# Kernel optimization log

Hardware: AMD Instinct MI355X
Metric: run time of the kernel (lower is better)

The kernel has to match this reference:

```python
import jax, jax.numpy as jnp
import numpy as np

B, T, E, H = 2, 2048, 1024, 16
HS = E // H  # head_size = 64
EPS = 1e-5


def _layernorm(x, g, b):
    mu = jnp.mean(x, axis=-1, keepdims=True)
    var = jnp.mean(jnp.square(x - mu), axis=-1, keepdims=True)
    return (x - mu) * jax.lax.rsqrt(var + EPS) * g + b


def _block_forward(x, wq, wk, wv, wp, bp, ln1_g, ln1_b, ln2_g, ln2_b,
                   w1, b1, w2, b2, w3, b3, wg_att, bg_att, wg_ff, bg_ff):
    Bc, Tc, Ec = x.shape
    # --- multi-head causal self-attention on ln1(x) ---
    h = _layernorm(x, ln1_g, ln1_b)
    q = jnp.einsum('bte,hek->bhtk', h, wq)  # [B,H,T,HS]
    k = jnp.einsum('bte,hek->bhtk', h, wk)
    v = jnp.einsum('bte,hek->bhtk', h, wv)
    scores = jnp.einsum('bhtk,bhsk->bhts', q, k) * (HS ** -0.5)
    causal = jnp.tril(jnp.ones((Tc, Tc), dtype=bool))
    scores = jnp.where(causal, scores, jnp.finfo(scores.dtype).min)
    wei = jax.nn.softmax(scores, axis=-1)  # [B,H,T,T] (returned, as in torch)
    attn = jnp.einsum('bhts,bhsk->bhtk', wei, v)
    # concat heads in head order -> [B,T,H*HS]
    attn = attn.transpose(0, 2, 1, 3).reshape(Bc, Tc, H * HS)
    sa_out = attn @ wp + bp
    # gated residual: gate from new value, multiply residual (old x)
    gate = jax.nn.sigmoid(sa_out @ wg_att + bg_att)
    x = sa_out + gate * x
    # --- feed-forward on ln2(x) ---
    h2 = _layernorm(x, ln2_g, ln2_b)
    f = jax.nn.gelu(h2 @ w1 + b1, approximate=False)   # [B,T,4E]
    f = jax.nn.gelu(f @ w2 + b2, approximate=False)    # [B,T,2E]
    f = f @ w3 + b3                                     # [B,T,E]
    gate2 = jax.nn.sigmoid(f @ wg_ff + bg_ff)
    x = f + gate2 * x
    return x, wei


def setup_inputs() -> dict:
    key = jax.random.key(0)
    ks = jax.random.split(key, 24)
    s = 0.02
    n = lambda i, shape: (jax.random.normal(ks[i], shape) * s).astype(jnp.float32)
    return {
        'x': jax.random.normal(ks[0], (B, T, E), dtype=jnp.float32),
        'wq': n(1, (H, E, HS)), 'wk': n(2, (H, E, HS)), 'wv': n(3, (H, E, HS)),
        'wp': n(4, (H * HS, E)), 'bp': jnp.zeros((E,), jnp.float32),
        'ln1_g': jnp.ones((E,), jnp.float32), 'ln1_b': jnp.zeros((E,), jnp.float32),
        'ln2_g': jnp.ones((E,), jnp.float32), 'ln2_b': jnp.zeros((E,), jnp.float32),
        'w1': n(5, (E, 4 * E)), 'b1': jnp.zeros((4 * E,), jnp.float32),
        'w2': n(6, (4 * E, 2 * E)), 'b2': jnp.zeros((2 * E,), jnp.float32),
        'w3': n(7, (2 * E, E)), 'b3': jnp.zeros((E,), jnp.float32),
        'wg_att': n(8, (E, E)), 'bg_att': jnp.zeros((E,), jnp.float32),
        'wg_ff': n(9, (E, E)), 'bg_ff': jnp.zeros((E,), jnp.float32),
    }


def reference(x, wq, wk, wv, wp, bp, ln1_g, ln1_b, ln2_g, ln2_b,
              w1, b1, w2, b2, w3, b3, wg_att, bg_att, wg_ff, bg_ff):
    return _block_forward(x, wq, wk, wv, wp, bp, ln1_g, ln1_b, ln2_g, ln2_b,
                          w1, b1, w2, b2, w3, b3, wg_att, bg_att, wg_ff, bg_ff)
```

## Files before the change

kernel.cpp:

```cpp
#include <hip/hip_runtime.h>
#include <hip/hip_bf16.h>

typedef unsigned short u16;
typedef __attribute__((ext_vector_type(8))) short short8;
typedef __attribute__((ext_vector_type(4))) float floatx4;

#define DI __device__ __forceinline__

constexpr int Tn  = 2048;
constexpr int En  = 1024;
constexpr int BTn = 4096;

DI float bf2f(u16 u) { union { unsigned int i; float f; } v; v.i = (unsigned int)u << 16; return v.f; }
DI u16 f2bf(float f) {
  union { float f; unsigned int i; } u; u.f = f;
  unsigned int r = u.i + 0x7FFFu + ((u.i >> 16) & 1u);
  return (u16)(r >> 16);
}
DI float gelu_f(float x) { return 0.5f * x * (1.f + erff(x * 0.70710678118654752f)); }
DI float sigmoid_f(float x) { return 1.f / (1.f + __expf(-x)); }

DI void gload_lds16(const u16* g, u16* l) {
  __builtin_amdgcn_global_load_lds(
      (const __attribute__((address_space(1))) unsigned int*)g,
      (__attribute__((address_space(3))) unsigned int*)l, 16, 0, 0);
}

template <int EPI>
__launch_bounds__(256, 2)
__global__ void gemm_bt(const u16* __restrict__ A, const u16* __restrict__ Bt,
                        const float* __restrict__ bias, u16* __restrict__ C,
                        int M, int N, int K) {
  __shared__ __align__(16) u16 As[128 * 32];
  __shared__ __align__(16) u16 Bs[128 * 32];
  const int tid = threadIdx.x;
  const int m0 = blockIdx.y << 7, n0 = blockIdx.x << 7;
  const int lane = tid & 63, l15 = lane & 15, quad = lane >> 4;
  const int wave = tid >> 6;
  const int wm = (wave >> 1) << 6, wn = (wave & 1) << 6;

  const int ra = tid >> 2, c8 = (tid & 3) << 3;
  const u16* pa0 = A + (size_t)(m0 + ra) * K + c8;
  const u16* pa1 = pa0 + (size_t)64 * K;
  const u16* pb0 = Bt + (size_t)(n0 + ra) * K + c8;
  const u16* pb1 = pb0 + (size_t)64 * K;
  u16* sA0 = &As[ra * 32 + c8]; u16* sA1 = &As[(ra + 64) * 32 + c8];
  u16* sB0 = &Bs[ra * 32 + c8]; u16* sB1 = &Bs[(ra + 64) * 32 + c8];

  floatx4 acc[4][4] = {};
  for (int k0 = 0; k0 < K; k0 += 32) {
    gload_lds16(pa0 + k0, sA0);
    gload_lds16(pa1 + k0, sA1);
    gload_lds16(pb0 + k0, sB0);
    gload_lds16(pb1 + k0, sB1);
    __syncthreads();
    short8 af[4], bfr[4];
#pragma unroll
    for (int i = 0; i < 4; ++i) {
      af[i]  = *(const short8*)&As[(wm + i * 16 + l15) * 32 + quad * 8];
      bfr[i] = *(const short8*)&Bs[(wn + i * 16 + l15) * 32 + quad * 8];
    }
#pragma unroll
    for (int i = 0; i < 4; ++i)
#pragma unroll
      for (int j = 0; j < 4; ++j)
        acc[i][j] = __builtin_amdgcn_mfma_f32_16x16x32_bf16(af[i], bfr[j], acc[i][j], 0, 0, 0);
    __syncthreads();
  }
#pragma unroll
  for (int j = 0; j < 4; ++j) {
    const int col = n0 + wn + j * 16 + l15;
    const float bv = bias ? bias[col] : 0.f;
#pragma unroll
    for (int i = 0; i < 4; ++i) {
#pragma unroll
      for (int r = 0; r < 4; ++r) {
        const int row = m0 + wm + i * 16 + quad * 4 + r;
        float v = acc[i][j][r] + bv;
        if (EPI == 1) v = gelu_f(v);
        if (EPI == 2) v = sigmoid_f(v);
        C[(size_t)row * N + col] = f2bf(v);
      }
    }
  }
}

__launch_bounds__(256, 2)
__global__ void attn_scores(const u16* __restrict__ qkv, float* __restrict__ wei,
                            float* __restrict__ lsum) {
  const int bh = blockIdx.z, b = bh >> 4, h = bh & 15;
  const int m0 = blockIdx.y << 7, n0 = blockIdx.x << 7;
  float* weib = wei + (size_t)bh * Tn * Tn;
  const int tid = threadIdx.x;
  if (n0 > m0 + 127) {
    const float4 z = {0.f, 0.f, 0.f, 0.f};
#pragma unroll
    for (int it = 0; it < 16; ++it) {
      int lin = it * 256 + tid;
      int r = lin >> 5, c4 = (lin & 31) << 2;
      *(float4*)&weib[(size_t)(m0 + r) * Tn + n0 + c4] = z;
    }
    return;
  }
  __shared__ __align__(16) u16 Qs[128 * 64];
  __shared__ __align__(16) u16 Ks[128 * 64];
  const int lane = tid & 63, l15 = lane & 15, quad = lane >> 4;
  const int wave = tid >> 6;
  const int wm = (wave >> 1) << 6, wn = (wave & 1) << 6;
  const u16* qb = qkv + (size_t)b * Tn * 3072 + h * 64;
  const u16* kb = qb + 1024;
#pragma unroll
  for (int it = 0; it < 4; ++it) {
    int lin = it * 256 + tid;
    int r = lin >> 3, cc = (lin & 7) << 3;
    gload_lds16(&qb[(size_t)(m0 + r) * 3072 + cc], &Qs[r * 64 + cc]);
    gload_lds16(&kb[(size_t)(n0 + r) * 3072 + cc], &Ks[r * 64 + cc]);
  }
  __syncthreads();
  floatx4 acc[4][4] = {};
#pragma unroll
  for (int ks = 0; ks < 2; ++ks) {
    short8 af[4], bfr[4];
#pragma unroll
    for (int i = 0; i < 4; ++i) {
      af[i]  = *(const short8*)&Qs[(wm + i * 16 + l15) * 64 + ks * 32 + quad * 8];
      bfr[i] = *(const short8*)&Ks[(wn + i * 16 + l15) * 64 + ks * 32 + quad * 8];
    }
#pragma unroll
    for (int i = 0; i < 4; ++i)
#pragma unroll
      for (int j = 0; j < 4; ++j)
        acc[i][j] = __builtin_amdgcn_mfma_f32_16x16x32_bf16(af[i], bfr[j], acc[i][j], 0, 0, 0);
  }
#pragma unroll
  for (int i = 0; i < 4; ++i) {
#pragma unroll
    for (int r = 0; r < 4; ++r) {
      const int row = m0 + wm + i * 16 + quad * 4 + r;
      float ps = 0.f;
#pragma unroll
      for (int j = 0; j < 4; ++j) {
        const int col = n0 + wn + j * 16 + l15;
        float p = (col <= row) ? __expf(acc[i][j][r] * 0.125f) : 0.f;
        weib[(size_t)row * Tn + col] = p;
        ps += p;
      }
      float v = ps;
      v += __shfl_xor(v, 1); v += __shfl_xor(v, 2);
      v += __shfl_xor(v, 4); v += __shfl_xor(v, 8);
      if (l15 == 0) atomicAdd(&lsum[bh * Tn + row], v);
    }
  }
}

__launch_bounds__(256, 2)
__global__ void attn_pv(float* __restrict__ wei, const u16* __restrict__ vT,
                        const float* __restrict__ lsum, u16* __restrict__ attn_out) {
  const int bh = blockIdx.z, b = bh >> 4, h = bh & 15;
  const int m0 = blockIdx.x << 7;
  float* weib = wei + (size_t)bh * Tn * Tn;
  const u16* vtb = vT + (size_t)bh * 64 * Tn;
  __shared__ __align__(16) u16 Ps[128 * 32];
  __shared__ __align__(16) u16 Vs[64 * 32];
  const int tid = threadIdx.x;
  const int lane = tid & 63, l15 = lane & 15, quad = lane >> 4;
  const int wave = tid >> 6;
  const int ra = tid >> 2, c8 = (tid & 3) << 3;
  const float inv0 = 1.f / lsum[bh * Tn + m0 + ra];
  const float inv1 = 1.f / lsum[bh * Tn + m0 + ra + 64];
  floatx4 acc[2][4] = {};
  const int kmax = m0 + 128;
  for (int k0 = 0; k0 < kmax; k0 += 32) {
    gload_lds16(&vtb[(size_t)ra * Tn + k0 + c8], &Vs[ra * 32 + c8]);
#pragma unroll
    for (int half = 0; half < 2; ++half) {
      const int r = ra + half * 64;
      const float inv = half ? inv1 : inv0;
      size_t go = (size_t)(m0 + r) * Tn + k0 + c8;
      float4 a = *(float4*)&weib[go];
      float4 b4 = *(float4*)&weib[go + 4];
      a.x *= inv; a.y *= inv; a.z *= inv; a.w *= inv;
      b4.x *= inv; b4.y *= inv; b4.z *= inv; b4.w *= inv;
      u16 o8[8] = { f2bf(a.x), f2bf(a.y), f2bf(a.z), f2bf(a.w),
                    f2bf(b4.x), f2bf(b4.y), f2bf(b4.z), f2bf(b4.w) };
      *(uint4*)&Ps[r * 32 + c8] = *(uint4*)o8;
      *(float4*)&weib[go] = a;
      *(float4*)&weib[go + 4] = b4;
    }
    __syncthreads();
    short8 af[2], bfr[4];
#pragma unroll
    for (int i = 0; i < 2; ++i)
      af[i] = *(const short8*)&Ps[(wave * 32 + i * 16 + l15) * 32 + quad * 8];
#pragma unroll
    for (int j = 0; j < 4; ++j)
      bfr[j] = *(const short8*)&Vs[(j * 16 + l15) * 32 + quad * 8];
#pragma unroll
    for (int i = 0; i < 2; ++i)
#pragma unroll
      for (int j = 0; j < 4; ++j)
        acc[i][j] = __builtin_amdgcn_mfma_f32_16x16x32_bf16(af[i], bfr[j], acc[i][j], 0, 0, 0);
    __syncthreads();
  }
#pragma unroll
  for (int i = 0; i < 2; ++i)
#pragma unroll
    for (int j = 0; j < 4; ++j)
#pragma unroll
      for (int r = 0; r < 4; ++r) {
        const int row = m0 + wave * 32 + i * 16 + quad * 4 + r;
        const int col = j * 16 + l15;
        attn_out[(size_t)(b * Tn + row) * En + h * 64 + col] = f2bf(acc[i][j][r]);
      }
}

__global__ void transpose_wf(const float* __restrict__ in, u16* __restrict__ out, int R, int Cc) {
  __shared__ u16 t[64][65];
  const int tid = threadIdx.x;
  const int r0 = blockIdx.y << 6, c0 = blockIdx.x << 6;
#pragma unroll
  for (int it = 0; it < 4; ++it) {
    int lin = it * 256 + tid;
    int r = lin >> 4, c4 = (lin & 15) << 2;
    float4 v = *(const float4*)&in[(size_t)(r0 + r) * Cc + c0 + c4];
    t[r][c4 + 0] = f2bf(v.x); t[r][c4 + 1] = f2bf(v.y);
    t[r][c4 + 2] = f2bf(v.z); t[r][c4 + 3] = f2bf(v.w);
  }
  __syncthreads();
#pragma unroll
  for (int it = 0; it < 2; ++it) {
    int lin = it * 256 + tid;
    int r = lin >> 3, cc = (lin & 7) << 3;
    u16 t8[8];
#pragma unroll
    for (int e = 0; e < 8; ++e) t8[e] = t[cc + e][r];
    *(uint4*)&out[(size_t)(c0 + r) * R + r0 + cc] = *(uint4*)t8;
  }
}

__global__ void repack_qkvw(const float* __restrict__ wq, const float* __restrict__ wk,
                            const float* __restrict__ wv, u16* __restrict__ out) {
  const int which = blockIdx.z;
  const float* w = which == 0 ? wq : (which == 1 ? wk : wv);
  const int h = blockIdx.y;
  const int e0 = blockIdx.x << 6;
  __shared__ u16 t[64][65];
  const int tid = threadIdx.x;
  const float* ib = w + (size_t)h * 1024 * 64;
#pragma unroll
  for (int it = 0; it < 4; ++it) {
    int lin = it * 256 + tid;
    int r = lin >> 4, c4 = (lin & 15) << 2;
    float4 v = *(const float4*)&ib[(size_t)(e0 + r) * 64 + c4];
    t[r][c4 + 0] = f2bf(v.x); t[r][c4 + 1] = f2bf(v.y);
    t[r][c4 + 2] = f2bf(v.z); t[r][c4 + 3] = f2bf(v.w);
  }
  __syncthreads();
  u16* ob = out + ((size_t)which * 1024 + h * 64) * 1024;
#pragma unroll
  for (int it = 0; it < 2; ++it) {
    int lin = it * 256 + tid;
    int r = lin >> 3, cc = (lin & 7) << 3;
    u16 t8[8];
#pragma unroll
    for (int e = 0; e < 8; ++e) t8[e] = t[cc + e][r];
    *(uint4*)&ob[(size_t)r * 1024 + e0 + cc] = *(uint4*)t8;
  }
}

__global__ void transpose_v(const u16* __restrict__ qkv, u16* __restrict__ vT) {
  const int bh = blockIdx.z, b = bh >> 4, h = bh & 15;
  const int s0 = blockIdx.x << 6;
  __shared__ u16 t[64][65];
  const int tid = threadIdx.x;
  const u16* ib = qkv + (size_t)b * Tn * 3072 + 2048 + h * 64;
#pragma unroll
  for (int it = 0; it < 2; ++it) {
    int lin = it * 256 + tid;
    int r = lin >> 3, cc = (lin & 7) << 3;
    uint4 v = *(const uint4*)&ib[(size_t)(s0 + r) * 3072 + cc];
    u16 t8[8]; *(uint4*)t8 = v;
#pragma unroll
    for (int e = 0; e < 8; ++e) t[r][cc + e] = t8[e];
  }
  __syncthreads();
  u16* ob = vT + (size_t)bh * 64 * Tn;
#pragma unroll
  for (int it = 0; it < 2; ++it) {
    int lin = it * 256 + tid;
    int r = lin >> 3, cc = (lin & 7) << 3;
    u16 t8[8];
#pragma unroll
    for (int e = 0; e < 8; ++e) t8[e] = t[cc + e][r];
    *(uint4*)&ob[(size_t)r * Tn + s0 + cc] = *(uint4*)t8;
  }
}

__launch_bounds__(256)
__global__ void layernorm_k(const float* __restrict__ x, const float* __restrict__ g,
                            const float* __restrict__ be, u16* __restrict__ out) {
  const int row = blockIdx.x;
  const int tid = threadIdx.x;
  const float* xr = x + (size_t)row * En;
  float4 xv = *(const float4*)&xr[tid * 4];
  float s = xv.x + xv.y + xv.z + xv.w;
  float sq = xv.x * xv.x + xv.y * xv.y + xv.z * xv.z + xv.w * xv.w;
#pragma unroll
  for (int o = 1; o < 64; o <<= 1) { s += __shfl_xor(s, o); sq += __shfl_xor(sq, o); }
  __shared__ float red[8];
  const int wave = tid >> 6, lane = tid & 63;
  if (lane == 0) { red[wave] = s; red[wave + 4] = sq; }
  __syncthreads();
  const float S  = red[0] + red[1] + red[2] + red[3];
  const float SQ = red[4] + red[5] + red[6] + red[7];
  const float mu = S * (1.f / 1024.f);
  const float var = SQ * (1.f / 1024.f) - mu * mu;
  const float rstd = rsqrtf(var + 1e-5f);
  float4 gv = *(const float4*)&g[tid * 4];
  float4 bv = *(const float4*)&be[tid * 4];
  ushort4 ov;
  ov.x = f2bf((xv.x - mu) * rstd * gv.x + bv.x);
  ov.y = f2bf((xv.y - mu) * rstd * gv.y + bv.y);
  ov.z = f2bf((xv.z - mu) * rstd * gv.z + bv.z);
  ov.w = f2bf((xv.w - mu) * rstd * gv.w + bv.w);
  *(ushort4*)&out[(size_t)row * En + tid * 4] = ov;
}

__global__ void gated_residual(const u16* __restrict__ val, const u16* __restrict__ gate,
                               const float* __restrict__ res, float* __restrict__ out) {
  const size_t i = ((size_t)blockIdx.x * 256 + threadIdx.x) * 4;
  ushort4 v = *(const ushort4*)&val[i];
  ushort4 g = *(const ushort4*)&gate[i];
  float4 r = *(const float4*)&res[i];
  float4 o;
  o.x = bf2f(v.x) + bf2f(g.x) * r.x;
  o.y = bf2f(v.y) + bf2f(g.y) * r.y;
  o.z = bf2f(v.z) + bf2f(g.z) * r.z;
  o.w = bf2f(v.w) + bf2f(g.w) * r.w;
  *(float4*)&out[i] = o;
}

extern "C" void kernel_launch(void* const* d_in, const int* in_sizes, int n_in,
                              void* d_out, int out_size, void* d_ws, size_t ws_size,
                              hipStream_t stream) {
  const float* x    = (const float*)d_in[0];
  const float* wq   = (const float*)d_in[1];
  const float* wk   = (const float*)d_in[2];
  const float* wv   = (const float*)d_in[3];
  const float* wp   = (const float*)d_in[4];
  const float* bp   = (const float*)d_in[5];
  const float* ln1g = (const float*)d_in[6];
  const float* ln1b = (const float*)d_in[7];
  const float* ln2g = (const float*)d_in[8];
  const float* ln2b = (const float*)d_in[9];
  const float* w1   = (const float*)d_in[10];
  const float* b1   = (const float*)d_in[11];
  const float* w2   = (const float*)d_in[12];
  const float* b2   = (const float*)d_in[13];
  const float* w3   = (const float*)d_in[14];
  const float* b3   = (const float*)d_in[15];
  const float* wga  = (const float*)d_in[16];
  const float* bga  = (const float*)d_in[17];
  const float* wgf  = (const float*)d_in[18];
  const float* bgf  = (const float*)d_in[19];

  float* out_x = (float*)d_out;
  float* wei   = out_x + (size_t)BTn * En;

  char* wsb = (char*)d_ws;
  size_t off = 0;
  auto alloc = [&](size_t bytes) { char* p = wsb + off; off += (bytes + 255) & ~(size_t)255; return p; };
  float* lsum = (float*)alloc((size_t)32 * Tn * 4);
  u16* WqkvT = (u16*)alloc((size_t)3072 * 1024 * 2);
  u16* wpT   = (u16*)alloc((size_t)1024 * 1024 * 2);
  u16* wgaT  = (u16*)alloc((size_t)1024 * 1024 * 2);
  u16* w1T   = (u16*)alloc((size_t)4096 * 1024 * 2);
  u16* w2T   = (u16*)alloc((size_t)2048 * 4096 * 2);
  u16* w3T   = (u16*)alloc((size_t)1024 * 2048 * 2);
  u16* wgfT  = (u16*)alloc((size_t)1024 * 1024 * 2);
  u16* h1    = (u16*)alloc((size_t)BTn * En * 2);
  u16* qkv   = (u16*)alloc((size_t)BTn * 3072 * 2);
  u16* vT    = (u16*)alloc((size_t)32 * 64 * Tn * 2);
  u16* attn  = (u16*)alloc((size_t)BTn * En * 2);
  u16* sa    = (u16*)alloc((size_t)BTn * En * 2);
  u16* glin  = (u16*)alloc((size_t)BTn * En * 2);
  float* x1  = (float*)alloc((size_t)BTn * En * 4);
  u16* h2 = h1;
  u16* f1 = qkv;
  u16* f2 = attn;
  u16* f3 = glin;
  u16* g2 = h1;

  hipMemsetAsync(lsum, 0, (size_t)32 * Tn * 4, stream);
  repack_qkvw<<<dim3(16, 16, 3), 256, 0, stream>>>(wq, wk, wv, WqkvT);
  transpose_wf<<<dim3(16, 16), 256, 0, stream>>>(wp,  wpT,  1024, 1024);
  transpose_wf<<<dim3(16, 16), 256, 0, stream>>>(wga, wgaT, 1024, 1024);
  transpose_wf<<<dim3(64, 16), 256, 0, stream>>>(w1,  w1T,  1024, 4096);
  transpose_wf<<<dim3(32, 64), 256, 0, stream>>>(w2,  w2T,  4096, 2048);
  transpose_wf<<<dim3(16, 32), 256, 0, stream>>>(w3,  w3T,  2048, 1024);
  transpose_wf<<<dim3(16, 16), 256, 0, stream>>>(wgf, wgfT, 1024, 1024);

  layernorm_k<<<BTn, 256, 0, stream>>>(x, ln1g, ln1b, h1);
  gemm_bt<0><<<dim3(24, 32), 256, 0, stream>>>(h1, WqkvT, nullptr, qkv, BTn, 3072, 1024);
  transpose_v<<<dim3(32, 1, 32), 256, 0, stream>>>(qkv, vT);
  attn_scores<<<dim3(16, 16, 32), 256, 0, stream>>>(qkv, wei, lsum);
  attn_pv<<<dim3(16, 1, 32), 256, 0, stream>>>(wei, vT, lsum, attn);
  gemm_bt<0><<<dim3(8, 32), 256, 0, stream>>>(attn, wpT, bp, sa, BTn, 1024, 1024);
  gemm_bt<2><<<dim3(8, 32), 256, 0, stream>>>(sa, wgaT, bga, glin, BTn, 1024, 1024);
  gated_residual<<<BTn, 256, 0, stream>>>(sa, glin, x, x1);
  layernorm_k<<<BTn, 256, 0, stream>>>(x1, ln2g, ln2b, h2);
  gemm_bt<1><<<dim3(32, 32), 256, 0, stream>>>(h2, w1T, b1, f1, BTn, 4096, 1024);
  gemm_bt<1><<<dim3(16, 32), 256, 0, stream>>>(f1, w2T, b2, f2, BTn, 2048, 4096);
  gemm_bt<0><<<dim3(8, 32), 256, 0, stream>>>(f2, w3T, b3, f3, BTn, 1024, 2048);
  gemm_bt<2><<<dim3(8, 32), 256, 0, stream>>>(f3, wgfT, bgf, g2, BTn, 1024, 1024);
  gated_residual<<<BTn, 256, 0, stream>>>(f3, g2, x1, out_x);
}
```

Before: 1.317 ms.

## Triple-buffer LDS tiles in bf16 GEMM with async global-to-LDS prefetch

Turns the single-buffered GEMM main loop into a three-stage pipeline. Tiles for the next three K steps are loaded into LDS ahead of use, and the loop waits on partial vmcnt counts so global loads overlap with MFMA compute. LDS use triples to 48KB per block, which may reduce occupancy under launch_bounds(256,2). The hand-written waitcnt values also depend on the exact count of outstanding loads.

After: 1.304 ms. No clear change (-1.0%).

```diff
diff --git a/kernel.cpp b/kernel.cpp
--- a/kernel.cpp
+++ b/kernel.cpp
@@ -31,8 +31,8 @@
 __global__ void gemm_bt(const u16* __restrict__ A, const u16* __restrict__ Bt,
                         const float* __restrict__ bias, u16* __restrict__ C,
                         int M, int N, int K) {
-  __shared__ __align__(16) u16 As[128 * 32];
-  __shared__ __align__(16) u16 Bs[128 * 32];
+  __shared__ __align__(16) u16 As[3][128 * 32];
+  __shared__ __align__(16) u16 Bs[3][128 * 32];
   const int tid = threadIdx.x;
   const int m0 = blockIdx.y << 7, n0 = blockIdx.x << 7;
   const int lane = tid & 63, l15 = lane & 15, quad = lane >> 4;
@@ -44,28 +44,45 @@
   const u16* pa1 = pa0 + (size_t)64 * K;
   const u16* pb0 = Bt + (size_t)(n0 + ra) * K + c8;
   const u16* pb1 = pb0 + (size_t)64 * K;
-  u16* sA0 = &As[ra * 32 + c8]; u16* sA1 = &As[(ra + 64) * 32 + c8];
-  u16* sB0 = &Bs[ra * 32 + c8]; u16* sB1 = &Bs[(ra + 64) * 32 + c8];
+  const int lo = ra * 32 + c8;
+
+  auto STG = [&](int b, int kt) {
+    const int ko = kt << 5;
+    gload_lds16(pa0 + ko, &As[b][lo]);
+    gload_lds16(pa1 + ko, &As[b][lo + 64 * 32]);
+    gload_lds16(pb0 + ko, &Bs[b][lo]);
+    gload_lds16(pb1 + ko, &Bs[b][lo + 64 * 32]);
+  };
+
+  const int nk = K >> 5;
+  STG(0, 0); STG(1, 1); STG(2, 2);
 
   floatx4 acc[4][4] = {};
-  for (int k0 = 0; k0 < K; k0 += 32) {
-    gload_lds16(pa0 + k0, sA0);
-    gload_lds16(pa1 + k0, sA1);
-    gload_lds16(pb0 + k0, sB0);
-    gload_lds16(pb1 + k0, sB1);
-    __syncthreads();
+  int cur = 0;
+  for (int k = 0; k < nk; ++k) {
+    const int rem = nk - k;
+    if (rem > 2)       asm volatile("s_waitcnt vmcnt(8)" ::: "memory");
+    else if (rem == 2) asm volatile("s_waitcnt vmcnt(4)" ::: "memory");
+    else               asm volatile("s_waitcnt vmcnt(0)" ::: "memory");
+    __builtin_amdgcn_s_barrier();
+    __builtin_amdgcn_sched_barrier(0);
+    const u16* Ab = As[cur];
+    const u16* Bb = Bs[cur];
     short8 af[4], bfr[4];
 #pragma unroll
     for (int i = 0; i < 4; ++i) {
-      af[i]  = *(const short8*)&As[(wm + i * 16 + l15) * 32 + quad * 8];
-      bfr[i] = *(const short8*)&Bs[(wn + i * 16 + l15) * 32 + quad * 8];
+      af[i]  = *(const short8*)&Ab[(wm + i * 16 + l15) * 32 + quad * 8];
+      bfr[i] = *(const short8*)&Bb[(wn + i * 16 + l15) * 32 + quad * 8];
     }
 #pragma unroll
     for (int i = 0; i < 4; ++i)
 #pragma unroll
       for (int j = 0; j < 4; ++j)
         acc[i][j] = __builtin_amdgcn_mfma_f32_16x16x32_bf16(af[i], bfr[j], acc[i][j], 0, 0, 0);
-    __syncthreads();
+    __builtin_amdgcn_s_barrier();
+    __builtin_amdgcn_sched_barrier(0);
+    if (k + 3 < nk) STG(cur, k + 3);
+    cur = (cur == 2) ? 0 : cur + 1;
   }
 #pragma unroll
   for (int j = 0; j < 4; ++j) {
```
